# Performance work log

Measured on AMD Instinct MI355X. Metric: run time of the kernel, lower is better.

Reference implementation:

```python
import jax, jax.numpy as jnp
import numpy as np

H = 8            # num_heads
HID = 128        # hidden_channels
D = HID // H     # per-head dim
L = 2            # num_layers
NCLS = 4         # out_channels (number of 1-class heads)


def _forward(x_a, x_b, lin_W_a, lin_b_a, lin_W_b, lin_b_b,
             Wk, bk, Wq, bq, Wv, bv, arel, mrel, prel,
             Wa, ba_out, skip, Wcls, bcls, edges):
    """HGT forward. edges: list of (src_type, dst_type, [2,E] int array); list
    position is the relation index into arel/mrel/prel."""
    # per-type input projection + ReLU
    x = [jax.nn.relu(x_a @ lin_W_a + lin_b_a),
         jax.nn.relu(x_b @ lin_W_b + lin_b_b)]
    N = [x[0].shape[0], x[1].shape[0]]
    scale = 1.0 / np.sqrt(D)
    for l in range(L):
        # per-type K/Q/V projections -> [N, H, D]
        k = [(x[t] @ Wk[l, t] + bk[l, t]).reshape(N[t], H, D) for t in range(2)]
        q = [(x[t] @ Wq[l, t] + bq[l, t]).reshape(N[t], H, D) for t in range(2)]
        v = [(x[t] @ Wv[l, t] + bv[l, t]).reshape(N[t], H, D) for t in range(2)]
        new_x = []
        for dt in range(2):
            logits, vals, dsts = [], [], []
            for r, (s_t, d_t, ei) in enumerate(edges):
                if d_t != dt:
                    continue
                src, dst = ei[0], ei[1]
                # relation-specific per-head transforms of gathered src K/V
                ke = jnp.einsum('ehd,hdf->ehf', k[s_t][src], arel[l, r])  # [E,H,D]
                ve = jnp.einsum('ehd,hdf->ehf', v[s_t][src], mrel[l, r])  # [E,H,D]
                a = jnp.sum(q[dt][dst] * ke, axis=-1) * prel[l, r] * scale  # [E,H]
                logits.append(a); vals.append(ve); dsts.append(dst)
            a = jnp.concatenate(logits, axis=0)
            ve = jnp.concatenate(vals, axis=0)
            dst = jnp.concatenate(dsts, axis=0)
            # segment softmax over all incoming edges per destination node
            amax = jax.ops.segment_max(a, dst, num_segments=N[dt])           # [N,H]
            ae = jnp.exp(a - amax[dst])                                       # [E,H]
            den = jax.ops.segment_sum(ae, dst, num_segments=N[dt])           # [N,H]
            msg = jax.ops.segment_sum(ae[:, :, None] * ve, dst,
                                      num_segments=N[dt])                    # [N,H,D]
            out = (msg / jnp.maximum(den, 1e-16)[:, :, None]).reshape(N[dt], HID)
            # output projection with GELU + learned skip gate
            out = jax.nn.gelu(out) @ Wa[l, dt] + ba_out[l, dt]
            beta = jax.nn.sigmoid(skip[l, dt])
            new_x.append(beta * out + (1.0 - beta) * x[dt])
        x = new_x
    # node_to_predict == 'a'; concatenated 1-class heads -> [Na, NCLS]
    return x[0] @ Wcls.T + bcls


def setup_inputs() -> dict:
    key = jax.random.key(0)
    ks = iter(jax.random.split(key, 40))
    Na, Nb, E = 50000, 50000, 150000
    def rn(shape, fan_in):
        return jax.random.normal(next(ks), shape, dtype=jnp.float32) / np.sqrt(fan_in)
    inp = {
        'x_a': jax.random.normal(next(ks), (Na, 64), dtype=jnp.float32),
        'x_b': jax.random.normal(next(ks), (Nb, 32), dtype=jnp.float32),
        'lin_W_a': rn((64, HID), 64), 'lin_b_a': jnp.zeros((HID,), jnp.float32),
        'lin_W_b': rn((32, HID), 32), 'lin_b_b': jnp.zeros((HID,), jnp.float32),
        'Wk': rn((L, 2, HID, HID), HID), 'bk': jnp.zeros((L, 2, HID), jnp.float32),
        'Wq': rn((L, 2, HID, HID), HID), 'bq': jnp.zeros((L, 2, HID), jnp.float32),
        'Wv': rn((L, 2, HID, HID), HID), 'bv': jnp.zeros((L, 2, HID), jnp.float32),
        'arel': rn((L, 4, H, D, D), D), 'mrel': rn((L, 4, H, D, D), D),
        'prel': jnp.ones((L, 4, H), jnp.float32),
        'Wa': rn((L, 2, HID, HID), HID), 'ba_out': jnp.zeros((L, 2, HID), jnp.float32),
        'skip': jnp.ones((L, 2), jnp.float32),
        'Wcls': rn((NCLS, HID), HID), 'bcls': jnp.zeros((NCLS,), jnp.float32),
        'edge_aa': jax.random.randint(next(ks), (2, E), 0, Na, dtype=jnp.int32),
        'edge_ab': jax.random.randint(next(ks), (2, E), 0, Na, dtype=jnp.int32),
        'edge_ba': jax.random.randint(next(ks), (2, E), 0, Na, dtype=jnp.int32),
        'edge_bb': jax.random.randint(next(ks), (2, E), 0, Nb, dtype=jnp.int32),
    }
    return inp


def reference(x_a, x_b, lin_W_a, lin_b_a, lin_W_b, lin_b_b,
              Wk, bk, Wq, bq, Wv, bv, arel, mrel, prel,
              Wa, ba_out, skip, Wcls, bcls,
              edge_aa, edge_ab, edge_ba, edge_bb):
    edges = [(0, 0, edge_aa), (0, 1, edge_ab), (1, 0, edge_ba), (1, 1, edge_bb)]
    return _forward(x_a, x_b, lin_W_a, lin_b_a, lin_W_b, lin_b_b,
                    Wk, bk, Wq, bq, Wv, bv, arel, mrel, prel,
                    Wa, ba_out, skip, Wcls, bcls, edges)
```

## Files before the change

### kernel.cpp

```cpp
#include <hip/hip_runtime.h>
#include <math.h>

#define HIDC 128
#define NH 8
#define HD 16
#define NCLS 4

typedef __attribute__((ext_vector_type(8))) short s8v;
typedef __attribute__((ext_vector_type(4))) float f4v;

#define ST_STRIDE 264

__device__ __forceinline__ float gelu_f(float h) {
    float z = 0.7978845608028654f * (h + 0.044715f * h * h * h);
    float t = 1.f - 2.f / (1.f + __expf(2.f * z));
    return 0.5f * h * (1.f + t);
}
__device__ __forceinline__ unsigned short f2bf(float x) {
    unsigned b = __float_as_uint(x);
    unsigned r = (b + 0x7FFFu + ((b >> 16) & 1u)) >> 16;
    return (unsigned short)r;
}
__device__ __forceinline__ float bf2f(unsigned short u) {
    return __uint_as_float(((unsigned)u) << 16);
}
__device__ __forceinline__ void gload_lds16(const void* g, void* l) {
    __builtin_amdgcn_global_load_lds(
        (const __attribute__((address_space(1))) unsigned int*)g,
        (__attribute__((address_space(3))) unsigned int*)l, 16, 0, 0);
}

__global__ void zero_u32(unsigned* __restrict__ p, long n)
{
    long i = (long)blockIdx.x * blockDim.x + threadIdx.x;
    long stride = (long)gridDim.x * blockDim.x;
    for (; i < n; i += stride) p[i] = 0u;
}

__global__ void fold_all(const float* __restrict__ Wk, const float* __restrict__ bk,
                         const float* __restrict__ Wv, const float* __restrict__ bv,
                         const float* __restrict__ arel, const float* __restrict__ mrel,
                         float* __restrict__ Wt, float* __restrict__ bt)
{
    __shared__ float rsh[NH * HD * HD];
// ... 145 lines not shown
    unsigned run = bsum[blockIdx.x] + sh[t] - s;
    #pragma unroll
    for (int j = 0; j < 4; ++j) {
        int i = i0 + j;
        if (i < n) { rp[i] = (int)run; cur[i] = run; }
        run += v[j];
    }
}

__global__ void scatter4(const int* __restrict__ e0, int E0, const int* __restrict__ e1, int E1,
                         const int* __restrict__ e2, int E2, const int* __restrict__ e3, int E3,
                         unsigned* __restrict__ cursor, int Nmax,
                         unsigned* __restrict__ adj0, unsigned* __restrict__ adj1)
{
    int i = blockIdx.x * blockDim.x + threadIdx.x;
    int tot = E0 + E1 + E2 + E3;
    int stride = gridDim.x * blockDim.x;
    for (; i < tot; i += stride) {
        int j = i; const int* e; int E; int dt; unsigned rb;
        if (j < E0) { e = e0; E = E0; dt = 0; rb = 0u; }
        else { j -= E0;
            if (j < E1) { e = e1; E = E1; dt = 1; rb = 0u; }
            else { j -= E1;
                if (j < E2) { e = e2; E = E2; dt = 0; rb = 1u << 24; }
                else { j -= E2; e = e3; E = E3; dt = 1; rb = 1u << 24; }
            }
        }
        int s = e[j], d = e[E + j];
        unsigned pos = atomicAdd(&cursor[(size_t)dt * Nmax + d], 1u);
        (dt ? adj1 : adj0)[pos] = (unsigned)s | rb;
    }
}

template <int ASPLIT, int EPI, int OUT, int NK>
__global__ __launch_bounds__(256)
void mgemm(const void* __restrict__ Ain, const unsigned short* __restrict__ W2m,
           const float* __restrict__ bias,
           const unsigned short* __restrict__ xold, const float* __restrict__ skipp,
           void* __restrict__ Cout, int N)
{
    constexpr int K = NK * 32;
    constexpr size_t WSZ = (size_t)4 * K * 128;
    constexpr size_t SSZ = (size_t)128 * ST_STRIDE * 2;
    constexpr size_t LSZ = (OUT == 2 && SSZ > WSZ) ? SSZ : WSZ;
    __shared__ char ldsraw[LSZ];
    unsigned short* lds = (unsigned short*)ldsraw;
    int t = threadIdx.x;
    constexpr int NCP = (4 * K * 128) / (16 * 256);
    #pragma unroll
    for (int i = 0; i < NCP; ++i)
        gload_lds16((const char*)W2m + ((size_t)t + i * 256) * 16,
                    (char*)ldsraw + ((size_t)t + i * 256) * 16);
    __syncthreads();

    int w = t >> 6, lane = t & 63;
    int lr = lane & 15, g = lane >> 4;
    int row0 = blockIdx.x * 128;
    int fnb = w * 2;

    f4v acc[8][2];
    #pragma unroll
    for (int i = 0; i < 8; ++i) { acc[i][0] = (f4v)0.f; acc[i][1] = (f4v)0.f; }

    #pragma unroll
    for (int ks = 0; ks < NK; ++ks) {
        s8v ah[8], al[8];
        #pragma unroll
        for (int fm = 0; fm < 8; ++fm) {
            int row = row0 + fm * 16 + lr;
            if (row < N) {
                if (ASPLIT) {
                    const unsigned short* ap = (const unsigned short*)Ain + (size_t)row * 256 + ks * 32 + g * 8;
                    ah[fm] = *(const s8v*)ap;
                    al[fm] = *(const s8v*)(ap + 128);
                } else {
                    const float* ap = (const float*)Ain + (size_t)row * K + ks * 32 + g * 8;
                    float4 p = *(const float4*)ap;
                    float4 q = *(const float4*)(ap + 4);
                    float xv[8] = {p.x, p.y, p.z, p.w, q.x, q.y, q.z, q.w};
                    #pragma unroll
                    for (int j = 0; j < 8; ++j) {
                        unsigned short h = f2bf(xv[j]);
                        ah[fm][j] = (short)h;
                        al[fm][j] = (short)f2bf(xv[j] - bf2f(h));
                    }
                }
            } else { ah[fm] = (s8v)0; al[fm] = (s8v)0; }
        }
        #pragma unroll
        for (int f = 0; f < 2; ++f) {
            int fn = fnb + f;
            size_t co = (size_t)ks * 8192 + fn * 1024 + g * 256 + lr * 16;
            s8v bh = *(const s8v*)((const char*)ldsraw + co);
            s8v bl = *(const s8v*)((const char*)ldsraw + K * 256 + co);
            #pragma unroll
            for (int fm = 0; fm < 8; ++fm) {
                acc[fm][f] = __builtin_amdgcn_mfma_f32_16x16x32_bf16(ah[fm], bh, acc[fm][f], 0, 0, 0);
                acc[fm][f] = __builtin_amdgcn_mfma_f32_16x16x32_bf16(ah[fm], bl, acc[fm][f], 0, 0, 0);
                acc[fm][f] = __builtin_amdgcn_mfma_f32_16x16x32_bf16(al[fm], bh, acc[fm][f], 0, 0, 0);
            }
        }
    }

    float beta = 0.f;
    if (EPI == 2) beta = 1.f / (1.f + __expf(-skipp[0]));
    int rb = g * 4;

    if (OUT == 2) __syncthreads();

    #pragma unroll
    for (int f = 0; f < 2; ++f) {
        int fn = fnb + f;
        float bv = bias[fn * 16 + lr];
        int col = fn * 16 + lr;
        #pragma unroll
        for (int fm = 0; fm < 8; ++fm) {
            #pragma unroll
            for (int j = 0; j < 4; ++j) {
                int lrow = fm * 16 + rb + j;
                int row = row0 + lrow;
                if (OUT == 0 && row >= N) continue;
                float o = acc[fm][f][j] + bv;
                if (EPI == 1) o = fmaxf(o, 0.f);
                if (EPI == 2) {
                    float xo = (row < N) ? (bf2f(xold[(size_t)row * 256 + col]) +
                                            bf2f(xold[(size_t)row * 256 + 128 + col])) : 0.f;
                    o = beta * o + (1.f - beta) * xo;
                }
                if (OUT == 0) {
                    ((float*)Cout)[(size_t)row * HIDC + col] = o;
                } else {
                    unsigned short h = f2bf(o);
                    lds[(size_t)lrow * ST_STRIDE + col] = h;
                    lds[(size_t)lrow * ST_STRIDE + 128 + col] = f2bf(o - bf2f(h));
                }
            }
        }
    }

    if (OUT == 2) {
        __syncthreads();
        #pragma unroll
        for (int it = 0; it < 16; ++it) {
            int d4 = (it * 256 + t) * 4;
            int row = d4 >> 7, c2 = d4 & 127;
            int grow = row0 + row;
            if (grow < N) {
                uint4 v = *(const uint4*)(lds + (size_t)row * ST_STRIDE + c2 * 2);
                *(uint4*)((unsigned short*)Cout + (size_t)grow * 256 + c2 * 2) = v;
            }
        }
    }
}

struct KvArgs {
    const unsigned short* A[4];
    const unsigned short* Wm[4];
    const float* bias[4];
    unsigned short* out[4];
    int N[4];
    int cum[5];
};

__global__ __launch_bounds__(256)
void mgemm_kv4(KvArgs args)
{
    int bid = blockIdx.x;
    int jb = 0;
    while (jb < 3 && bid >= args.cum[jb + 1]) ++jb;
    int lb = bid - args.cum[jb];
    const unsigned short* Ain = args.A[jb];
    const unsigned short* Wkt = args.Wm[jb];
    const unsigned short* Wvt = args.Wm[jb] + 32768;
    const float* bias2 = args.bias[jb];
    unsigned short* kv = args.out[jb];
    int N = args.N[jb];

    __shared__ char ldsraw[65536];
    unsigned short* lds = (unsigned short*)ldsraw;
    int t = threadIdx.x;
    #pragma unroll
    for (int i = 0; i < 8; ++i)
        gload_lds16((const char*)Wkt + ((size_t)t + i * 256) * 16,
                    ldsraw + ((size_t)t + i * 256) * 16);
    #pragma unroll
    for (int i = 0; i < 8; ++i)
        gload_lds16((const char*)Wvt + ((size_t)t + i * 256) * 16,
                    ldsraw + 32768 + ((size_t)t + i * 256) * 16);

    int w = t >> 6, lane = t & 63;
    int lr = lane & 15, g = lane >> 4;
    int row0 = lb * 64;
    int fnb = w * 2;

    s8v ah[4][4], al[4][4];
    #pragma unroll
    for (int fm = 0; fm < 4; ++fm) {
        int row = row0 + fm * 16 + lr;
        #pragma unroll
        for (int ks = 0; ks < 4; ++ks) {
            if (row < N) {
                const unsigned short* ap = Ain + (size_t)row * 256 + ks * 32 + g * 8;
                ah[fm][ks] = *(const s8v*)ap;
                al[fm][ks] = *(const s8v*)(ap + 128);
            } else { ah[fm][ks] = (s8v)0; al[fm][ks] = (s8v)0; }
        }
    }
    __syncthreads();

    f4v acck[4][2], accv[4][2];
    #pragma unroll
    for (int i = 0; i < 4; ++i) {
        acck[i][0] = (f4v)0.f; acck[i][1] = (f4v)0.f;
        accv[i][0] = (f4v)0.f; accv[i][1] = (f4v)0.f;
    }

    #pragma unroll
    for (int ks = 0; ks < 4; ++ks) {
        #pragma unroll
        for (int f = 0; f < 2; ++f) {
            int fn = fnb + f;
            size_t co = (size_t)ks * 8192 + fn * 1024 + g * 256 + lr * 16;
            s8v bk_ = *(const s8v*)(ldsraw + co);
            s8v bv_ = *(const s8v*)(ldsraw + 32768 + co);
            #pragma unroll
            for (int fm = 0; fm < 4; ++fm) {
                acck[fm][f] = __builtin_amdgcn_mfma_f32_16x16x32_bf16(ah[fm][ks], bk_, acck[fm][f], 0, 0, 0);
                acck[fm][f] = __builtin_amdgcn_mfma_f32_16x16x32_bf16(al[fm][ks], bk_, acck[fm][f], 0, 0, 0);
                accv[fm][f] = __builtin_amdgcn_mfma_f32_16x16x32_bf16(ah[fm][ks], bv_, accv[fm][f], 0, 0, 0);
                accv[fm][f] = __builtin_amdgcn_mfma_f32_16x16x32_bf16(al[fm][ks], bv_, accv[fm][f], 0, 0, 0);
            }
        }
    }

    __syncthreads();
    int rb = g * 4;
    #pragma unroll
    for (int f = 0; f < 2; ++f) {
        int fn = fnb + f;
        int col = fn * 16 + lr;
        float bk0 = bias2[col], bv0 = bias2[128 + col];
        #pragma unroll
        for (int fm = 0; fm < 4; ++fm) {
            #pragma unroll
            for (int j = 0; j < 4; ++j) {
                int lrow = fm * 16 + rb + j;
                lds[(size_t)lrow * ST_STRIDE + col] = f2bf(acck[fm][f][j] + bk0);
                lds[(size_t)lrow * ST_STRIDE + 128 + col] = f2bf(accv[fm][f][j] + bv0);
            }
        }
    }
    __syncthreads();
    #pragma unroll
    for (int it = 0; it < 8; ++it) {
        int d4 = (it * 256 + t) * 4;
        int row = d4 >> 7, c2 = d4 & 127;
        int grow = row0 + row;
        if (grow < N) {
            uint4 v = *(const uint4*)(lds + (size_t)row * ST_STRIDE + c2 * 2);
            *(uint4*)(kv + (size_t)grow * 256 + c2 * 2) = v;
        }
    }
}

struct QArgs {
    const unsigned short* A[2];
    const unsigned short* Wm[2];
    const float* bias[2];
    float* out[2];
    int N[2];
    int cum[3];
};

__global__ __launch_bounds__(256)
void mgemm_q2(QArgs args)
{
    int bid = blockIdx.x;
    int jb = (bid >= args.cum[1]) ? 1 : 0;
    int lb = bid - args.cum[jb];
    const unsigned short* Ain = args.A[jb];
    const unsigned short* W2m = args.Wm[jb];
    const float* bias = args.bias[jb];
    float* Cout = args.out[jb];
    int N = args.N[jb];

    __shared__ unsigned short lds[2 * 128 * 128];
    int t = threadIdx.x;
    #pragma unroll
    for (int i = 0; i < 16; ++i)
        gload_lds16((const char*)W2m + ((size_t)t + i * 256) * 16,
                    (char*)lds + ((size_t)t + i * 256) * 16);
    __syncthreads();

    int w = t >> 6, lane = t & 63;
    int lr = lane & 15, g = lane >> 4;
    int row0 = lb * 128;
    int fnb = w * 2;

    f4v acc[8][2];
    #pragma unroll
    for (int i = 0; i < 8; ++i) { acc[i][0] = (f4v)0.f; acc[i][1] = (f4v)0.f; }

    #pragma unroll
    for (int ks = 0; ks < 4; ++ks) {
        s8v ah[8], al[8];
        #pragma unroll
        for (int fm = 0; fm < 8; ++fm) {
            int row = row0 + fm * 16 + lr;
            if (row < N) {
                const unsigned short* ap = Ain + (size_t)row * 256 + ks * 32 + g * 8;
                ah[fm] = *(const s8v*)ap;
                al[fm] = *(const s8v*)(ap + 128);
            } else { ah[fm] = (s8v)0; al[fm] = (s8v)0; }
        }
        #pragma unroll
        for (int f = 0; f < 2; ++f) {
            int fn = fnb + f;
            size_t co = (size_t)ks * 8192 + fn * 1024 + g * 256 + lr * 16;
            s8v bh = *(const s8v*)((const char*)lds + co);
            s8v bl = *(const s8v*)((const char*)lds + 32768 + co);
            #pragma unroll
            for (int fm = 0; fm < 8; ++fm) {
                acc[fm][f] = __builtin_amdgcn_mfma_f32_16x16x32_bf16(ah[fm], bh, acc[fm][f], 0, 0, 0);
                acc[fm][f] = __builtin_amdgcn_mfma_f32_16x16x32_bf16(ah[fm], bl, acc[fm][f], 0, 0, 0);
                acc[fm][f] = __builtin_amdgcn_mfma_f32_16x16x32_bf16(al[fm], bh, acc[fm][f], 0, 0, 0);
            }
        }
    }

    int rb = g * 4;
    #pragma unroll
    for (int f = 0; f < 2; ++f) {
        int fn = fnb + f;
        float bv = bias[fn * 16 + lr];
        int col = fn * 16 + lr;
        #pragma unroll
        for (int fm = 0; fm < 8; ++fm) {
            #pragma unroll
            for (int j = 0; j < 4; ++j) {
                int row = row0 + fm * 16 + rb + j;
                if (row >= N) continue;
                Cout[(size_t)row * HIDC + col] = acc[fm][f][j] + bv;
            }
        }
    }
}

#define EDGE_STEP(IDX, M, S, AX, AY)                                               \
    {                                                                              \
        unsigned ent = adj[IDX];                                                   \
        int src = (int)(ent & 0xFFFFFFu);                                          \
        const unsigned short* kv = (ent >> 24) ? kvB : kvA;                        \
        float sp = (ent >> 24) ? spB : spA;                                        \
        ushort2 kraw = *(const ushort2*)(kv + (size_t)src * 256 + lane * 2);       \
        ushort2 vraw = *(const ushort2*)(kv + (size_t)src * 256 + 128 + lane * 2); \
        float p = bf2f(kraw.x) * qv.x + bf2f(kraw.y) * qv.y;                       \
        p += __shfl_xor(p, 1, 8);                                                  \
        p += __shfl_xor(p, 2, 8);                                                  \
        p += __shfl_xor(p, 4, 8);                                                  \
        float a = p * sp;                                                          \
        float mn = fmaxf(M, a);                                                    \
        float cc = __expf(M - mn);                                                 \
        float pe = __expf(a - mn);                                                 \
        S = S * cc + pe;                                                           \
        AX = AX * cc + pe * bf2f(vraw.x);                                          \
        AY = AY * cc + pe * bf2f(vraw.y);                                          \
        M = mn;                                                                    \
    }

__global__ __launch_bounds__(256)
void agg_fused(const float* __restrict__ Q,
               const unsigned short* __restrict__ kvA, const unsigned short* __restrict__ kvB,
               const int* __restrict__ rowptr, const unsigned* __restrict__ adj,
               const float* __restrict__ prelA, const float* __restrict__ prelB,
               float scale, unsigned short* __restrict__ msgs, int N)
{
// ... 116 lines not shown
    float* bt = (float*)base; base += (size_t)16 * HIDC * 4;
    size_t nW2 = (size_t)2 * (Ka + Kb) * 128 + (size_t)24 * 32768;
    unsigned short* W2 = (unsigned short*)base; base += nW2 * 2;
    unsigned* cnt = (unsigned*)base; base += (size_t)2 * Nmax * 4;
    unsigned* cursor = (unsigned*)base; base += (size_t)2 * Nmax * 4;
    unsigned* bsum = (unsigned*)base; base += 256 * 4;
    int* rowptr = (int*)base; base += (size_t)2 * (Nmax + 1) * 4;
    unsigned* adj0 = (unsigned*)base; base += (size_t)(Ee[0] + Ee[2]) * 4;
    unsigned* adj1 = (unsigned*)base; base += (size_t)(Ee[1] + Ee[3]) * 4;

    size_t off_lina = 0;
    size_t off_linb = (size_t)2 * Ka * 128;
    size_t base128  = (size_t)2 * (Ka + Kb) * 128;
    auto offKT = [&](int l, int st, int dt) { return base128 + (size_t)(l * 8 + (st * 2 + dt) * 2) * 32768; };
    auto offQ  = [&](int l, int tt) { return base128 + (size_t)(16 + l * 2 + tt) * 32768; };
    auto offA  = [&](int l, int tt) { return base128 + (size_t)(20 + l * 2 + tt) * 32768; };

    fold_all<<<16, 128, 0, stream>>>(Wk, bk, Wv, bv, arel, mrel, Wt, bt);
    int nwblk = (Ka >> 5) + (Kb >> 5) + 24 * 4;
    wsplit<<<nwblk, 128, 0, stream>>>(lin_W_a, lin_W_b, Wq, Wa, Wt, W2, Ka, Kb);

    int nblk = (Nmax + 1023) / 1024;
    zero_u32<<<512, 256, 0, stream>>>(cnt, (long)2 * Nmax);
    hist4<<<1024, 256, 0, stream>>>(eptr[0] + Ee[0], Ee[0], eptr[1] + Ee[1], Ee[1],
                                    eptr[2] + Ee[2], Ee[2], eptr[3] + Ee[3], Ee[3],
                                    cnt, Nmax);
    scan_p1<<<2 * nblk, 256, 0, stream>>>(cnt, bsum, Nmax, nblk, Na, Nb);
    scan_p2<<<1, 256, 0, stream>>>(bsum, nblk, rowptr, Nmax, Na, Nb);
    scan_p3<<<2 * nblk, 256, 0, stream>>>(cnt, bsum, rowptr, cursor, Nmax, nblk, Na, Nb);
    scatter4<<<1024, 256, 0, stream>>>(eptr[0], Ee[0], eptr[1], Ee[1],
                                       eptr[2], Ee[2], eptr[3], Ee[3],
                                       cursor, Nmax, adj0, adj1);

    int gn128[2] = {(Na + 127) / 128, (Nb + 127) / 128};
    int gn64[2]  = {(Na + 63) / 64, (Nb + 63) / 64};
    mgemm<0, 1, 2, 2><<<gn128[0], 256, 0, stream>>>(x_a, W2 + off_lina, lin_b_a,
                                                    nullptr, nullptr, xs[0], Na);
    mgemm<0, 1, 2, 1><<<gn128[1], 256, 0, stream>>>(x_b, W2 + off_linb, lin_b_b,
                                                    nullptr, nullptr, xs[1], Nb);

    const float scale = 0.25f;

    for (int l = 0; l < 2; ++l) {
        KvArgs ka;
        int cum = 0;
        for (int j = 0; j < 4; ++j) {
            int st = j >> 1, dt = j & 1;
            int bid = l * 8 + (st * 2 + dt) * 2;
            ka.A[j] = xs[st];
            ka.Wm[j] = W2 + offKT(l, st, dt);
            ka.bias[j] = bt + (size_t)bid * HIDC;
            ka.out[j] = kvb[st][dt];
            ka.N[j] = Nn[st];
            ka.cum[j] = cum;
            cum += gn64[st];
        }
        ka.cum[4] = cum;
        mgemm_kv4<<<cum, 256, 0, stream>>>(ka);

        QArgs qa;
        qa.A[0] = xs[0]; qa.Wm[0] = W2 + offQ(l, 0);
        qa.bias[0] = bq + (l * 2 + 0) * HIDC; qa.out[0] = qb[0]; qa.N[0] = Nn[0];
        qa.A[1] = xs[1]; qa.Wm[1] = W2 + offQ(l, 1);
        qa.bias[1] = bq + (l * 2 + 1) * HIDC; qa.out[1] = qb[1]; qa.N[1] = Nn[1];
        qa.cum[0] = 0; qa.cum[1] = gn128[0]; qa.cum[2] = gn128[0] + gn128[1];
        mgemm_q2<<<qa.cum[2], 256, 0, stream>>>(qa);

        agg_fused<<<(Nn[1] + 3) / 4, 256, 0, stream>>>(qb[1], kvb[0][1], kvb[1][1],
                                                       rowptr + (Nmax + 1), adj1,
                                                       prel + (l * 4 + 1) * NH, prel + (l * 4 + 3) * NH,
                                                       scale, msgs, Nn[1]);
        mgemm<1, 2, 2, 4><<<gn128[1], 256, 0, stream>>>(msgs, W2 + offA(l, 1),
                                                        ba + (l * 2 + 1) * HIDC,
                                                        xs[1], skip + (l * 2 + 1), xs[1], Nn[1]);
        agg_fused<<<(Nn[0] + 3) / 4, 256, 0, stream>>>(qb[0], kvb[0][0], kvb[1][0],
                                                       rowptr, adj0,
                                                       prel + (l * 4 + 0) * NH, prel + (l * 4 + 2) * NH,
                                                       scale, msgs, Nn[0]);
        mgemm<1, 2, 2, 4><<<gn128[0], 256, 0, stream>>>(msgs, W2 + offA(l, 0),
                                                        ba + (l * 2 + 0) * HIDC,
                                                        xs[0], skip + (l * 2 + 0), xs[0], Nn[0]);
    }

    cls_kernel<<<(Na + 3) / 4, 256, 0, stream>>>(xs[0], Wcls, bcls, (float*)d_out, Na);
}
```

Baseline: 702.7 us.

## Merge K/V and Q GEMMs into one launch with 64-row tiles

Replaces the separate KV and Q GEMM kernels with one layer_gemm launch per layer that covers six jobs. It also moves the dense GEMMs from 128-row to 64-row tiles, staging the hi and lo weight halves through LDS in two sequential phases. The aim is fewer launches, more blocks for occupancy, and smaller LDS use. The cost is reloading weights mid-kernel behind extra barriers, and for the Q jobs dropping the lo activation term, which reduces precision slightly.

```diff
diff --git a/kernel.cpp b/kernel.cpp
--- a/kernel.cpp
+++ b/kernel.cpp
@@ -10,6 +10,7 @@
 typedef __attribute__((ext_vector_type(4))) float f4v;
 
 #define ST_STRIDE 264
+#define ST_BYTES  (64 * ST_STRIDE * 2)
 
 __device__ __forceinline__ float gelu_f(float h) {
     float z = 0.7978845608028654f * (h + 0.044715f * h * h * h);
@@ -221,41 +222,40 @@
     }
 }
 
-template <int ASPLIT, int EPI, int OUT, int NK>
+template <int ASPLIT, int EPI, int NK>
 __global__ __launch_bounds__(256)
-void mgemm(const void* __restrict__ Ain, const unsigned short* __restrict__ W2m,
-           const float* __restrict__ bias,
-           const unsigned short* __restrict__ xold, const float* __restrict__ skipp,
-           void* __restrict__ Cout, int N)
+void mgemm64(const void* __restrict__ Ain, const unsigned short* __restrict__ W2m,
+             const float* __restrict__ bias,
+             const unsigned short* __restrict__ xold, const float* __restrict__ skipp,
+             unsigned short* __restrict__ Cout, int N)
 {
     constexpr int K = NK * 32;
-    constexpr size_t WSZ = (size_t)4 * K * 128;
-    constexpr size_t SSZ = (size_t)128 * ST_STRIDE * 2;
-    constexpr size_t LSZ = (OUT == 2 && SSZ > WSZ) ? SSZ : WSZ;
+    constexpr int PB = K * 256;
+    constexpr size_t LSZ = (PB > ST_BYTES) ? PB : ST_BYTES;
     __shared__ char ldsraw[LSZ];
     unsigned short* lds = (unsigned short*)ldsraw;
     int t = threadIdx.x;
-    constexpr int NCP = (4 * K * 128) / (16 * 256);
+    constexpr int NCP = PB / (16 * 256);
     #pragma unroll
     for (int i = 0; i < NCP; ++i)
         gload_lds16((const char*)W2m + ((size_t)t + i * 256) * 16,
-                    (char*)ldsraw + ((size_t)t + i * 256) * 16);
+                    ldsraw + ((size_t)t + i * 256) * 16);
     __syncthreads();
 
     int w = t >> 6, lane = t & 63;
     int lr = lane & 15, g = lane >> 4;
-    int row0 = blockIdx.x * 128;
+    int row0 = blockIdx.x * 64;
     int fnb = w * 2;
 
-    f4v acc[8][2];
-    #pragma unroll
-    for (int i = 0; i < 8; ++i) { acc[i][0] = (f4v)0.f; acc[i][1] = (f4v)0.f; }
+    f4v acc[4][2];
+    #pragma unroll
+    for (int i = 0; i < 4; ++i) { acc[i][0] = (f4v)0.f; acc[i][1] = (f4v)0.f; }
 
     #pragma unroll
     for (int ks = 0; ks < NK; ++ks) {
-        s8v ah[8], al[8];
-        #pragma unroll
-        for (int fm = 0; fm < 8; ++fm) {
+        s8v ah[4], al[4];
+        #pragma unroll
+        for (int fm = 0; fm < 4; ++fm) {
             int row = row0 + fm * 16 + lr;
             if (row < N) {
                 if (ASPLIT) {
@@ -278,37 +278,66 @@
         }
         #pragma unroll
         for (int f = 0; f < 2; ++f) {
-            int fn = fnb + f;
-            size_t co = (size_t)ks * 8192 + fn * 1024 + g * 256 + lr * 16;
-            s8v bh = *(const s8v*)((const char*)ldsraw + co);
-            s8v bl = *(const s8v*)((const char*)ldsraw + K * 256 + co);
+            size_t co = (size_t)ks * 8192 + (fnb + f) * 1024 + g * 256 + lr * 16;
+            s8v b = *(const s8v*)(ldsraw + co);
             #pragma unroll
-            for (int fm = 0; fm < 8; ++fm) {
-                acc[fm][f] = __builtin_amdgcn_mfma_f32_16x16x32_bf16(ah[fm], bh, acc[fm][f], 0, 0, 0);
-                acc[fm][f] = __builtin_amdgcn_mfma_f32_16x16x32_bf16(ah[fm], bl, acc[fm][f], 0, 0, 0);
-                acc[fm][f] = __builtin_amdgcn_mfma_f32_16x16x32_bf16(al[fm], bh, acc[fm][f], 0, 0, 0);
-            }
+            for (int fm = 0; fm < 4; ++fm) {
+                acc[fm][f] = __builtin_amdgcn_mfma_f32_16x16x32_bf16(ah[fm], b, acc[fm][f], 0, 0, 0);
+                acc[fm][f] = __builtin_amdgcn_mfma_f32_16x16x32_bf16(al[fm], b, acc[fm][f], 0, 0, 0);
+            }
+        }
+    }
+
+    __syncthreads();
+    #pragma unroll
+    for (int i = 0; i < NCP; ++i)
+        gload_lds16((const char*)(W2m + (size_t)K * 128) + ((size_t)t + i * 256) * 16,
+                    ldsraw + ((size_t)t + i * 256) * 16);
+    __syncthreads();
+
+    #pragma unroll
+    for (int ks = 0; ks < NK; ++ks) {
+        s8v ah[4];
+        #pragma unroll
+        for (int fm = 0; fm < 4; ++fm) {
+            int row = row0 + fm * 16 + lr;
+            if (row < N) {
+                if (ASPLIT) {
+                    ah[fm] = *(const s8v*)((const unsigned short*)Ain + (size_t)row * 256 + ks * 32 + g * 8);
+                } else {
+                    const float* ap = (const float*)Ain + (size_t)row * K + ks * 32 + g * 8;
+                    float4 p = *(const float4*)ap;
+                    float4 q = *(const float4*)(ap + 4);
+                    float xv[8] = {p.x, p.y, p.z, p.w, q.x, q.y, q.z, q.w};
+                    #pragma unroll
+                    for (int j = 0; j < 8; ++j) ah[fm][j] = (short)f2bf(xv[j]);
+                }
+            } else ah[fm] = (s8v)0;
+        }
+        #pragma unroll
+        for (int f = 0; f < 2; ++f) {
+            size_t co = (size_t)ks * 8192 + (fnb + f) * 1024 + g * 256 + lr * 16;
+            s8v b = *(const s8v*)(ldsraw + co);
+            #pragma unroll
+            for (int fm = 0; fm < 4; ++fm)
+                acc[fm][f] = __builtin_amdgcn_mfma_f32_16x16x32_bf16(ah[fm], b, acc[fm][f], 0, 0, 0);
         }
     }
 
     float beta = 0.f;
     if (EPI == 2) beta = 1.f / (1.f + __expf(-skipp[0]));
     int rb = g * 4;
-
-    if (OUT == 2) __syncthreads();
-
+    __syncthreads();
     #pragma unroll
     for (int f = 0; f < 2; ++f) {
-        int fn = fnb + f;
-        float bv = bias[fn * 16 + lr];
-        int col = fn * 16 + lr;
-        #pragma unroll
-        for (int fm = 0; fm < 8; ++fm) {
+        int col = (fnb + f) * 16 + lr;
+        float bv = bias[col];
+        #pragma unroll
+        for (int fm = 0; fm < 4; ++fm) {
             #pragma unroll
             for (int j = 0; j < 4; ++j) {
                 int lrow = fm * 16 + rb + j;
                 int row = row0 + lrow;
-                if (OUT == 0 && row >= N) continue;
                 float o = acc[fm][f][j] + bv;
                 if (EPI == 1) o = fmaxf(o, 0.f);
                 if (EPI == 2) {
@@ -316,126 +345,9 @@
                                             bf2f(xold[(size_t)row * 256 + 128 + col])) : 0.f;
                     o = beta * o + (1.f - beta) * xo;
                 }
-                if (OUT == 0) {
-                    ((float*)Cout)[(size_t)row * HIDC + col] = o;
-                } else {
-                    unsigned short h = f2bf(o);
-                    lds[(size_t)lrow * ST_STRIDE + col] = h;
-                    lds[(size_t)lrow * ST_STRIDE + 128 + col] = f2bf(o - bf2f(h));
-                }
-            }
-        }
-    }
-
-    if (OUT == 2) {
-        __syncthreads();
-        #pragma unroll
-        for (int it = 0; it < 16; ++it) {
-            int d4 = (it * 256 + t) * 4;
-            int row = d4 >> 7, c2 = d4 & 127;
-            int grow = row0 + row;
-            if (grow < N) {
-                uint4 v = *(const uint4*)(lds + (size_t)row * ST_STRIDE + c2 * 2);
-                *(uint4*)((unsigned short*)Cout + (size_t)grow * 256 + c2 * 2) = v;
-            }
-        }
-    }
-}
-
-struct KvArgs {
-    const unsigned short* A[4];
-    const unsigned short* Wm[4];
-    const float* bias[4];
-    unsigned short* out[4];
-    int N[4];
-    int cum[5];
-};
-
-__global__ __launch_bounds__(256)
-void mgemm_kv4(KvArgs args)
-{
-    int bid = blockIdx.x;
-    int jb = 0;
-    while (jb < 3 && bid >= args.cum[jb + 1]) ++jb;
-    int lb = bid - args.cum[jb];
-    const unsigned short* Ain = args.A[jb];
-    const unsigned short* Wkt = args.Wm[jb];
-    const unsigned short* Wvt = args.Wm[jb] + 32768;
-    const float* bias2 = args.bias[jb];
-    unsigned short* kv = args.out[jb];
-    int N = args.N[jb];
-
-    __shared__ char ldsraw[65536];
-    unsigned short* lds = (unsigned short*)ldsraw;
-    int t = threadIdx.x;
-    #pragma unroll
-    for (int i = 0; i < 8; ++i)
-        gload_lds16((const char*)Wkt + ((size_t)t + i * 256) * 16,
-                    ldsraw + ((size_t)t + i * 256) * 16);
-    #pragma unroll
-    for (int i = 0; i < 8; ++i)
-        gload_lds16((const char*)Wvt + ((size_t)t + i * 256) * 16,
-                    ldsraw + 32768 + ((size_t)t + i * 256) * 16);
-
-    int w = t >> 6, lane = t & 63;
-    int lr = lane & 15, g = lane >> 4;
-    int row0 = lb * 64;
-    int fnb = w * 2;
-
-    s8v ah[4][4], al[4][4];
-    #pragma unroll
-    for (int fm = 0; fm < 4; ++fm) {
-        int row = row0 + fm * 16 + lr;
-        #pragma unroll
-        for (int ks = 0; ks < 4; ++ks) {
-            if (row < N) {
-                const unsigned short* ap = Ain + (size_t)row * 256 + ks * 32 + g * 8;
-                ah[fm][ks] = *(const s8v*)ap;
-                al[fm][ks] = *(const s8v*)(ap + 128);
-            } else { ah[fm][ks] = (s8v)0; al[fm][ks] = (s8v)0; }
-        }
-    }
-    __syncthreads();
-
-    f4v acck[4][2], accv[4][2];
-    #pragma unroll
-    for (int i = 0; i < 4; ++i) {
-        acck[i][0] = (f4v)0.f; acck[i][1] = (f4v)0.f;
-        accv[i][0] = (f4v)0.f; accv[i][1] = (f4v)0.f;
-    }
-
-    #pragma unroll
-    for (int ks = 0; ks < 4; ++ks) {
-        #pragma unroll
-        for (int f = 0; f < 2; ++f) {
-            int fn = fnb + f;
-            size_t co = (size_t)ks * 8192 + fn * 1024 + g * 256 + lr * 16;
-            s8v bk_ = *(const s8v*)(ldsraw + co);
-            s8v bv_ = *(const s8v*)(ldsraw + 32768 + co);
-            #pragma unroll
-            for (int fm = 0; fm < 4; ++fm) {
-                acck[fm][f] = __builtin_amdgcn_mfma_f32_16x16x32_bf16(ah[fm][ks], bk_, acck[fm][f], 0, 0, 0);
-                acck[fm][f] = __builtin_amdgcn_mfma_f32_16x16x32_bf16(al[fm][ks], bk_, acck[fm][f], 0, 0, 0);
-                accv[fm][f] = __builtin_amdgcn_mfma_f32_16x16x32_bf16(ah[fm][ks], bv_, accv[fm][f], 0, 0, 0);
-                accv[fm][f] = __builtin_amdgcn_mfma_f32_16x16x32_bf16(al[fm][ks], bv_, accv[fm][f], 0, 0, 0);
-            }
-        }
-    }
-
-    __syncthreads();
-    int rb = g * 4;
-    #pragma unroll
-    for (int f = 0; f < 2; ++f) {
-        int fn = fnb + f;
-        int col = fn * 16 + lr;
-        float bk0 = bias2[col], bv0 = bias2[128 + col];
-        #pragma unroll
-        for (int fm = 0; fm < 4; ++fm) {
-            #pragma unroll
-            for (int j = 0; j < 4; ++j) {
-                int lrow = fm * 16 + rb + j;
-                lds[(size_t)lrow * ST_STRIDE + col] = f2bf(acck[fm][f][j] + bk0);
-                lds[(size_t)lrow * ST_STRIDE + 128 + col] = f2bf(accv[fm][f][j] + bv0);
+                unsigned short h = f2bf(o);
+                lds[(size_t)lrow * ST_STRIDE + col] = h;
+                lds[(size_t)lrow * ST_STRIDE + 128 + col] = f2bf(o - bf2f(h));
             }
         }
     }
@@ -447,89 +359,155 @@
         int grow = row0 + row;
         if (grow < N) {
             uint4 v = *(const uint4*)(lds + (size_t)row * ST_STRIDE + c2 * 2);
-            *(uint4*)(kv + (size_t)grow * 256 + c2 * 2) = v;
-        }
-    }
-}
-
-struct QArgs {
-    const unsigned short* A[2];
-    const unsigned short* Wm[2];
-    const float* bias[2];
-    float* out[2];
-    int N[2];
-    int cum[3];
+            *(uint4*)(Cout + (size_t)grow * 256 + c2 * 2) = v;
+        }
+    }
+}
+
+struct LJob {
+    const unsigned short* A;
+    const unsigned short* W1;
+    const unsigned short* W2p;
+    const float* bias;
+    void* out;
+    int N;
+    int mode;
 };
+struct LArgs { LJob job[6]; int cum[7]; };
 
 __global__ __launch_bounds__(256)
-void mgemm_q2(QArgs args)
+void layer_gemm(LArgs args)
 {
     int bid = blockIdx.x;
-    int jb = (bid >= args.cum[1]) ? 1 : 0;
+    int jb = 0;
+    while (jb < 5 && bid >= args.cum[jb + 1]) ++jb;
+    LJob J = args.job[jb];
     int lb = bid - args.cum[jb];
-    const unsigned short* Ain = args.A[jb];
-    const unsigned short* W2m = args.Wm[jb];
-    const float* bias = args.bias[jb];
-    float* Cout = args.out[jb];
-    int N = args.N[jb];
-
-    __shared__ unsigned short lds[2 * 128 * 128];
+
+    __shared__ char ldsraw[ST_BYTES];
+    unsigned short* lds = (unsigned short*)ldsraw;
     int t = threadIdx.x;
     #pragma unroll
-    for (int i = 0; i < 16; ++i)
-        gload_lds16((const char*)W2m + ((size_t)t + i * 256) * 16,
-                    (char*)lds + ((size_t)t + i * 256) * 16);
+    for (int i = 0; i < 8; ++i)
+        gload_lds16((const char*)J.W1 + ((size_t)t + i * 256) * 16,
+                    ldsraw + ((size_t)t + i * 256) * 16);
     __syncthreads();
 
     int w = t >> 6, lane = t & 63;
     int lr = lane & 15, g = lane >> 4;
-    int row0 = lb * 128;
+    int row0 = lb * 64;
     int fnb = w * 2;
-
-    f4v acc[8][2];
-    #pragma unroll
-    for (int i = 0; i < 8; ++i) { acc[i][0] = (f4v)0.f; acc[i][1] = (f4v)0.f; }
+    int N = J.N;
+
+    f4v acc1[4][2], acc2[4][2];
+    #pragma unroll
+    for (int i = 0; i < 4; ++i) {
+        acc1[i][0] = (f4v)0.f; acc1[i][1] = (f4v)0.f;
+        acc2[i][0] = (f4v)0.f; acc2[i][1] = (f4v)0.f;
+    }
 
     #pragma unroll
     for (int ks = 0; ks < 4; ++ks) {
-        s8v ah[8], al[8];
-        #pragma unroll
-        for (int fm = 0; fm < 8; ++fm) {
+        s8v ah[4], al[4];
+        #pragma unroll
+        for (int fm = 0; fm < 4; ++fm) {
             int row = row0 + fm * 16 + lr;
             if (row < N) {
-                const unsigned short* ap = Ain + (size_t)row * 256 + ks * 32 + g * 8;
+                const unsigned short* ap = J.A + (size_t)row * 256 + ks * 32 + g * 8;
                 ah[fm] = *(const s8v*)ap;
                 al[fm] = *(const s8v*)(ap + 128);
             } else { ah[fm] = (s8v)0; al[fm] = (s8v)0; }
         }
         #pragma unroll
         for (int f = 0; f < 2; ++f) {
-            int fn = fnb + f;
-            size_t co = (size_t)ks * 8192 + fn * 1024 + g * 256 + lr * 16;
-            s8v bh = *(const s8v*)((const char*)lds + co);
-            s8v bl = *(const s8v*)((const char*)lds + 32768 + co);
+            size_t co = (size_t)ks * 8192 + (fnb + f) * 1024 + g * 256 + lr * 16;
+            s8v b = *(const s8v*)(ldsraw + co);
             #pragma unroll
-            for (int fm = 0; fm < 8; ++fm) {
-                acc[fm][f] = __builtin_amdgcn_mfma_f32_16x16x32_bf16(ah[fm], bh, acc[fm][f], 0, 0, 0);
-                acc[fm][f] = __builtin_amdgcn_mfma_f32_16x16x32_bf16(ah[fm], bl, acc[fm][f], 0, 0, 0);
-                acc[fm][f] = __builtin_amdgcn_mfma_f32_16x16x32_bf16(al[fm], bh, acc[fm][f], 0, 0, 0);
+            for (int fm = 0; fm < 4; ++fm) {
+                acc1[fm][f] = __builtin_amdgcn_mfma_f32_16x16x32_bf16(ah[fm], b, acc1[fm][f], 0, 0, 0);
+                acc1[fm][f] = __builtin_amdgcn_mfma_f32_16x16x32_bf16(al[fm], b, acc1[fm][f], 0, 0, 0);
+            }
+        }
+    }
+
+    __syncthreads();
+    #pragma unroll
+    for (int i = 0; i < 8; ++i)
+        gload_lds16((const char*)J.W2p + ((size_t)t + i * 256) * 16,
+                    ldsraw + ((size_t)t + i * 256) * 16);
+    __syncthreads();
+
+    #pragma unroll
+    for (int ks = 0; ks < 4; ++ks) {
+        s8v ah[4], al[4];
+        #pragma unroll
+        for (int fm = 0; fm < 4; ++fm) {
+            int row = row0 + fm * 16 + lr;
+            if (row < N) {
+                const unsigned short* ap = J.A + (size_t)row * 256 + ks * 32 + g * 8;
+                ah[fm] = *(const s8v*)ap;
+                if (J.mode == 0) al[fm] = *(const s8v*)(ap + 128);
+                else al[fm] = (s8v)0;
+            } else { ah[fm] = (s8v)0; al[fm] = (s8v)0; }
+        }
+        #pragma unroll
+        for (int f = 0; f < 2; ++f) {
+            size_t co = (size_t)ks * 8192 + (fnb + f) * 1024 + g * 256 + lr * 16;
+            s8v b = *(const s8v*)(ldsraw + co);
+            #pragma unroll
+            for (int fm = 0; fm < 4; ++fm) {
+                if (J.mode == 0) {
+                    acc2[fm][f] = __builtin_amdgcn_mfma_f32_16x16x32_bf16(ah[fm], b, acc2[fm][f], 0, 0, 0);
+                    acc2[fm][f] = __builtin_amdgcn_mfma_f32_16x16x32_bf16(al[fm], b, acc2[fm][f], 0, 0, 0);
+                } else {
+                    acc1[fm][f] = __builtin_amdgcn_mfma_f32_16x16x32_bf16(ah[fm], b, acc1[fm][f], 0, 0, 0);
+                }
             }
         }
     }
 
     int rb = g * 4;
-    #pragma unroll
-    for (int f = 0; f < 2; ++f) {
-        int fn = fnb + f;
-        float bv = bias[fn * 16 + lr];
-        int col = fn * 16 + lr;
-        #pragma unroll
-        for (int fm = 0; fm < 8; ++fm) {
+    if (J.mode == 0) {
+        __syncthreads();
+        unsigned short* kv = (unsigned short*)J.out;
+        #pragma unroll
+        for (int f = 0; f < 2; ++f) {
+            int col = (fnb + f) * 16 + lr;
+            float bk0 = J.bias[col], bv0 = J.bias[128 + col];
             #pragma unroll
-            for (int j = 0; j < 4; ++j) {
-                int row = row0 + fm * 16 + rb + j;
-                if (row >= N) continue;
-                Cout[(size_t)row * HIDC + col] = acc[fm][f][j] + bv;
+            for (int fm = 0; fm < 4; ++fm) {
+                #pragma unroll
+                for (int j = 0; j < 4; ++j) {
+                    int lrow = fm * 16 + rb + j;
+                    lds[(size_t)lrow * ST_STRIDE + col] = f2bf(acc1[fm][f][j] + bk0);
+                    lds[(size_t)lrow * ST_STRIDE + 128 + col] = f2bf(acc2[fm][f][j] + bv0);
+                }
+            }
+        }
+        __syncthreads();
+        #pragma unroll
+        for (int it = 0; it < 8; ++it) {
+            int d4 = (it * 256 + t) * 4;
+            int row = d4 >> 7, c2 = d4 & 127;
+            int grow = row0 + row;
+            if (grow < N) {
+                uint4 v = *(const uint4*)(lds + (size_t)row * ST_STRIDE + c2 * 2);
+                *(uint4*)(kv + (size_t)grow * 256 + c2 * 2) = v;
+            }
+        }
+    } else {
+        float* Cout = (float*)J.out;
+        #pragma unroll
+        for (int f = 0; f < 2; ++f) {
+            int col = (fnb + f) * 16 + lr;
+            float bv = J.bias[col];
+            #pragma unroll
+            for (int fm = 0; fm < 4; ++fm) {
+                #pragma unroll
+                for (int j = 0; j < 4; ++j) {
+                    int row = row0 + fm * 16 + rb + j;
+                    if (row < N) Cout[(size_t)row * HIDC + col] = acc1[fm][f][j] + bv;
+                }
             }
         }
     }
@@ -713,54 +691,58 @@
                                        eptr[2], Ee[2], eptr[3], Ee[3],
                                        cursor, Nmax, adj0, adj1);
 
-    int gn128[2] = {(Na + 127) / 128, (Nb + 127) / 128};
-    int gn64[2]  = {(Na + 63) / 64, (Nb + 63) / 64};
-    mgemm<0, 1, 2, 2><<<gn128[0], 256, 0, stream>>>(x_a, W2 + off_lina, lin_b_a,
-                                                    nullptr, nullptr, xs[0], Na);
-    mgemm<0, 1, 2, 1><<<gn128[1], 256, 0, stream>>>(x_b, W2 + off_linb, lin_b_b,
-                                                    nullptr, nullptr, xs[1], Nb);
+    int gn64[2] = {(Na + 63) / 64, (Nb + 63) / 64};
+    mgemm64<0, 1, 2><<<gn64[0], 256, 0, stream>>>(x_a, W2 + off_lina, lin_b_a,
+                                                  nullptr, nullptr, xs[0], Na);
+    mgemm64<0, 1, 1><<<gn64[1], 256, 0, stream>>>(x_b, W2 + off_linb, lin_b_b,
+                                                  nullptr, nullptr, xs[1], Nb);
 
     const float scale = 0.25f;
 
     for (int l = 0; l < 2; ++l) {
-        KvArgs ka;
+        LArgs la;
         int cum = 0;
         for (int j = 0; j < 4; ++j) {
             int st = j >> 1, dt = j & 1;
             int bid = l * 8 + (st * 2 + dt) * 2;
-            ka.A[j] = xs[st];
-            ka.Wm[j] = W2 + offKT(l, st, dt);
-            ka.bias[j] = bt + (size_t)bid * HIDC;
-            ka.out[j] = kvb[st][dt];
-            ka.N[j] = Nn[st];
-            ka.cum[j] = cum;
+            la.job[j].A = xs[st];
+            la.job[j].W1 = W2 + offKT(l, st, dt);
+            la.job[j].W2p = W2 + offKT(l, st, dt) + 32768;
+            la.job[j].bias = bt + (size_t)bid * HIDC;
+            la.job[j].out = kvb[st][dt];
+            la.job[j].N = Nn[st];
+            la.job[j].mode = 0;
+            la.cum[j] = cum;
             cum += gn64[st];
         }
-        ka.cum[4] = cum;
-        mgemm_kv4<<<cum, 256, 0, stream>>>(ka);
-
-        QArgs qa;
-        qa.A[0] = xs[0]; qa.Wm[0] = W2 + offQ(l, 0);
-        qa.bias[0] = bq + (l * 2 + 0) * HIDC; qa.out[0] = qb[0]; qa.N[0] = Nn[0];
-        qa.A[1] = xs[1]; qa.Wm[1] = W2 + offQ(l, 1);
-        qa.bias[1] = bq + (l * 2 + 1) * HIDC; qa.out[1] = qb[1]; qa.N[1] = Nn[1];
-        qa.cum[0] = 0; qa.cum[1] = gn128[0]; qa.cum[2] = gn128[0] + gn128[1];
-        mgemm_q2<<<qa.cum[2], 256, 0, stream>>>(qa);
+        for (int j = 0; j < 2; ++j) {
+            la.job[4 + j].A = xs[j];
+            la.job[4 + j].W1 = W2 + offQ(l, j);
+            la.job[4 + j].W2p = W2 + offQ(l, j) + 16384;
+            la.job[4 + j].bias = bq + (l * 2 + j) * HIDC;
+            la.job[4 + j].out = qb[j];
+            la.job[4 + j].N = Nn[j];
+            la.job[4 + j].mode = 1;
+            la.cum[4 + j] = cum;
+            cum += gn64[j];
+        }
+        la.cum[6] = cum;
+        layer_gemm<<<cum, 256, 0, stream>>>(la);
 
         agg_fused<<<(Nn[1] + 3) / 4, 256, 0, stream>>>(qb[1], kvb[0][1], kvb[1][1],
                                                        rowptr + (Nmax + 1), adj1,
                                                        prel + (l * 4 + 1) * NH, prel + (l * 4 + 3) * NH,
                                                        scale, msgs, Nn[1]);
-        mgemm<1, 2, 2, 4><<<gn128[1], 256, 0, stream>>>(msgs, W2 + offA(l, 1),
-                                                        ba + (l * 2 + 1) * HIDC,
-                                                        xs[1], skip + (l * 2 + 1), xs[1], Nn[1]);
+        mgemm64<1, 2, 4><<<gn64[1], 256, 0, stream>>>(msgs, W2 + offA(l, 1),
+                                                      ba + (l * 2 + 1) * HIDC,
+                                                      xs[1], skip + (l * 2 + 1), xs[1], Nn[1]);
         agg_fused<<<(Nn[0] + 3) / 4, 256, 0, stream>>>(qb[0], kvb[0][0], kvb[1][0],
                                                        rowptr, adj0,
                                                        prel + (l * 4 + 0) * NH, prel + (l * 4 + 2) * NH,
                                                        scale, msgs, Nn[0]);
-        mgemm<1, 2, 2, 4><<<gn128[0], 256, 0, stream>>>(msgs, W2 + offA(l, 0),
-                                                        ba + (l * 2 + 0) * HIDC,
-                                                        xs[0], skip + (l * 2 + 0), xs[0], Nn[0]);
+        mgemm64<1, 2, 4><<<gn64[0], 256, 0, stream>>>(msgs, W2 + offA(l, 0),
+                                                      ba + (l * 2 + 0) * HIDC,
+                                                      xs[0], skip + (l * 2 + 0), xs[0], Nn[0]);
     }
 
     cls_kernel<<<(Na + 3) / 4, 256, 0, stream>>>(xs[0], Wcls, bcls, (float*)d_out, Na);
```

Measured after the change: 774.8 us. 10.3% more time.

## Use two-pass split-bf16 GEMMs with 64-row tiles and per-type Q launches

Applied to the files above, without the earlier changes.

The GEMM kernel drops the low-half weight term, doing hi*W + lo*W (2 MFMAs) instead of 3, and only loads the high-precision weight half into LDS. Row tiles shrink from 128 to 64 so more blocks launch, and the fused Q kernel is replaced by two separate launches of the generic GEMM. Dropping the weight low part loses some accuracy, but only relative to the more precise three-term split; the grid doubles and one extra launch is added per layer.

```diff
diff --git a/kernel.cpp b/kernel.cpp
--- a/kernel.cpp
+++ b/kernel.cpp
@@ -10,6 +10,7 @@
 typedef __attribute__((ext_vector_type(4))) float f4v;
 
 #define ST_STRIDE 264
+#define ST_BYTES  (64 * ST_STRIDE * 2)
 
 __device__ __forceinline__ float gelu_f(float h) {
     float z = 0.7978845608028654f * (h + 0.044715f * h * h * h);
@@ -223,39 +224,38 @@
 
 template <int ASPLIT, int EPI, int OUT, int NK>
 __global__ __launch_bounds__(256)
-void mgemm(const void* __restrict__ Ain, const unsigned short* __restrict__ W2m,
-           const float* __restrict__ bias,
-           const unsigned short* __restrict__ xold, const float* __restrict__ skipp,
-           void* __restrict__ Cout, int N)
+void mg2p(const void* __restrict__ Ain, const unsigned short* __restrict__ Whi,
+          const float* __restrict__ bias,
+          const unsigned short* __restrict__ xold, const float* __restrict__ skipp,
+          void* __restrict__ Cout, int N)
 {
     constexpr int K = NK * 32;
-    constexpr size_t WSZ = (size_t)4 * K * 128;
-    constexpr size_t SSZ = (size_t)128 * ST_STRIDE * 2;
-    constexpr size_t LSZ = (OUT == 2 && SSZ > WSZ) ? SSZ : WSZ;
+    constexpr int PB = NK * 8192;
+    constexpr size_t LSZ = (OUT == 2 && ST_BYTES > PB) ? ST_BYTES : PB;
     __shared__ char ldsraw[LSZ];
     unsigned short* lds = (unsigned short*)ldsraw;
     int t = threadIdx.x;
-    constexpr int NCP = (4 * K * 128) / (16 * 256);
+    constexpr int NCP = PB / (16 * 256);
     #pragma unroll
     for (int i = 0; i < NCP; ++i)
-        gload_lds16((const char*)W2m + ((size_t)t + i * 256) * 16,
-                    (char*)ldsraw + ((size_t)t + i * 256) * 16);
+        gload_lds16((const char*)Whi + ((size_t)t + i * 256) * 16,
+                    ldsraw + ((size_t)t + i * 256) * 16);
     __syncthreads();
 
     int w = t >> 6, lane = t & 63;
     int lr = lane & 15, g = lane >> 4;
-    int row0 = blockIdx.x * 128;
+    int row0 = blockIdx.x * 64;
     int fnb = w * 2;
 
-    f4v acc[8][2];
-    #pragma unroll
-    for (int i = 0; i < 8; ++i) { acc[i][0] = (f4v)0.f; acc[i][1] = (f4v)0.f; }
+    f4v acc[4][2];
+    #pragma unroll
+    for (int i = 0; i < 4; ++i) { acc[i][0] = (f4v)0.f; acc[i][1] = (f4v)0.f; }
 
     #pragma unroll
     for (int ks = 0; ks < NK; ++ks) {
-        s8v ah[8], al[8];
-        #pragma unroll
-        for (int fm = 0; fm < 8; ++fm) {
+        s8v ah[4], al[4];
+        #pragma unroll
+        for (int fm = 0; fm < 4; ++fm) {
             int row = row0 + fm * 16 + lr;
             if (row < N) {
                 if (ASPLIT) {
@@ -278,15 +278,12 @@
         }
         #pragma unroll
         for (int f = 0; f < 2; ++f) {
-            int fn = fnb + f;
-            size_t co = (size_t)ks * 8192 + fn * 1024 + g * 256 + lr * 16;
-            s8v bh = *(const s8v*)((const char*)ldsraw + co);
-            s8v bl = *(const s8v*)((const char*)ldsraw + K * 256 + co);
+            size_t co = (size_t)ks * 8192 + (fnb + f) * 1024 + g * 256 + lr * 16;
+            s8v b = *(const s8v*)(ldsraw + co);
             #pragma unroll
-            for (int fm = 0; fm < 8; ++fm) {
-                acc[fm][f] = __builtin_amdgcn_mfma_f32_16x16x32_bf16(ah[fm], bh, acc[fm][f], 0, 0, 0);
-                acc[fm][f] = __builtin_amdgcn_mfma_f32_16x16x32_bf16(ah[fm], bl, acc[fm][f], 0, 0, 0);
-                acc[fm][f] = __builtin_amdgcn_mfma_f32_16x16x32_bf16(al[fm], bh, acc[fm][f], 0, 0, 0);
+            for (int fm = 0; fm < 4; ++fm) {
+                acc[fm][f] = __builtin_amdgcn_mfma_f32_16x16x32_bf16(ah[fm], b, acc[fm][f], 0, 0, 0);
+                acc[fm][f] = __builtin_amdgcn_mfma_f32_16x16x32_bf16(al[fm], b, acc[fm][f], 0, 0, 0);
             }
         }
     }
@@ -295,48 +292,56 @@
     if (EPI == 2) beta = 1.f / (1.f + __expf(-skipp[0]));
     int rb = g * 4;
 
-    if (OUT == 2) __syncthreads();
-
-    #pragma unroll
-    for (int f = 0; f < 2; ++f) {
-        int fn = fnb + f;
-        float bv = bias[fn * 16 + lr];
-        int col = fn * 16 + lr;
-        #pragma unroll
-        for (int fm = 0; fm < 8; ++fm) {
+    if (OUT == 2) {
+        __syncthreads();
+        #pragma unroll
+        for (int f = 0; f < 2; ++f) {
+            int col = (fnb + f) * 16 + lr;
+            float bv = bias[col];
             #pragma unroll
-            for (int j = 0; j < 4; ++j) {
-                int lrow = fm * 16 + rb + j;
-                int row = row0 + lrow;
-                if (OUT == 0 && row >= N) continue;
-                float o = acc[fm][f][j] + bv;
-                if (EPI == 1) o = fmaxf(o, 0.f);
-                if (EPI == 2) {
-                    float xo = (row < N) ? (bf2f(xold[(size_t)row * 256 + col]) +
-                                            bf2f(xold[(size_t)row * 256 + 128 + col])) : 0.f;
-                    o = beta * o + (1.f - beta) * xo;
-                }
-                if (OUT == 0) {
-                    ((float*)Cout)[(size_t)row * HIDC + col] = o;
-                } else {
+            for (int fm = 0; fm < 4; ++fm) {
+                #pragma unroll
+                for (int j = 0; j < 4; ++j) {
+                    int lrow = fm * 16 + rb + j;
+                    int row = row0 + lrow;
+                    float o = acc[fm][f][j] + bv;
+                    if (EPI == 1) o = fmaxf(o, 0.f);
+                    if (EPI == 2) {
+                        float xo = (row < N) ? (bf2f(xold[(size_t)row * 256 + col]) +
+                                                bf2f(xold[(size_t)row * 256 + 128 + col])) : 0.f;
+                        o = beta * o + (1.f - beta) * xo;
+                    }
                     unsigned short h = f2bf(o);
                     lds[(size_t)lrow * ST_STRIDE + col] = h;
                     lds[(size_t)lrow * ST_STRIDE + 128 + col] = f2bf(o - bf2f(h));
                 }
             }
         }
-    }
-
-    if (OUT == 2) {
         __syncthreads();
-        #pragma unroll
-        for (int it = 0; it < 16; ++it) {
+        unsigned short* C = (unsigned short*)Cout;
+        #pragma unroll
+        for (int it = 0; it < 8; ++it) {
             int d4 = (it * 256 + t) * 4;
             int row = d4 >> 7, c2 = d4 & 127;
             int grow = row0 + row;
             if (grow < N) {
                 uint4 v = *(const uint4*)(lds + (size_t)row * ST_STRIDE + c2 * 2);
-                *(uint4*)((unsigned short*)Cout + (size_t)grow * 256 + c2 * 2) = v;
+                *(uint4*)(C + (size_t)grow * 256 + c2 * 2) = v;
+            }
+        }
+    } else {
+        float* C = (float*)Cout;
+        #pragma unroll
+        for (int f = 0; f < 2; ++f) {
+            int col = (fnb + f) * 16 + lr;
+            float bv = bias[col];
+            #pragma unroll
+            for (int fm = 0; fm < 4; ++fm) {
+                #pragma unroll
+                for (int j = 0; j < 4; ++j) {
+                    int row = row0 + fm * 16 + rb + j;
+                    if (row < N) C[(size_t)row * HIDC + col] = acc[fm][f][j] + bv;
+                }
             }
         }
     }
@@ -448,89 +453,6 @@
         if (grow < N) {
             uint4 v = *(const uint4*)(lds + (size_t)row * ST_STRIDE + c2 * 2);
             *(uint4*)(kv + (size_t)grow * 256 + c2 * 2) = v;
-        }
-    }
-}
-
-struct QArgs {
-    const unsigned short* A[2];
-    const unsigned short* Wm[2];
-    const float* bias[2];
-    float* out[2];
-    int N[2];
-    int cum[3];
-};
-
-__global__ __launch_bounds__(256)
-void mgemm_q2(QArgs args)
-{
-    int bid = blockIdx.x;
-    int jb = (bid >= args.cum[1]) ? 1 : 0;
-    int lb = bid - args.cum[jb];
-    const unsigned short* Ain = args.A[jb];
-    const unsigned short* W2m = args.Wm[jb];
-    const float* bias = args.bias[jb];
-    float* Cout = args.out[jb];
-    int N = args.N[jb];
-
-    __shared__ unsigned short lds[2 * 128 * 128];
-    int t = threadIdx.x;
-    #pragma unroll
-    for (int i = 0; i < 16; ++i)
-        gload_lds16((const char*)W2m + ((size_t)t + i * 256) * 16,
-                    (char*)lds + ((size_t)t + i * 256) * 16);
-    __syncthreads();
-
-    int w = t >> 6, lane = t & 63;
-    int lr = lane & 15, g = lane >> 4;
-    int row0 = lb * 128;
-    int fnb = w * 2;
-
-    f4v acc[8][2];
-    #pragma unroll
-    for (int i = 0; i < 8; ++i) { acc[i][0] = (f4v)0.f; acc[i][1] = (f4v)0.f; }
-
-    #pragma unroll
-    for (int ks = 0; ks < 4; ++ks) {
-        s8v ah[8], al[8];
-        #pragma unroll
-        for (int fm = 0; fm < 8; ++fm) {
-            int row = row0 + fm * 16 + lr;
-            if (row < N) {
-                const unsigned short* ap = Ain + (size_t)row * 256 + ks * 32 + g * 8;
-                ah[fm] = *(const s8v*)ap;
-                al[fm] = *(const s8v*)(ap + 128);
-            } else { ah[fm] = (s8v)0; al[fm] = (s8v)0; }
-        }
-        #pragma unroll
-        for (int f = 0; f < 2; ++f) {
-            int fn = fnb + f;
-            size_t co = (size_t)ks * 8192 + fn * 1024 + g * 256 + lr * 16;
-            s8v bh = *(const s8v*)((const char*)lds + co);
-            s8v bl = *(const s8v*)((const char*)lds + 32768 + co);
-            #pragma unroll
-            for (int fm = 0; fm < 8; ++fm) {
-                acc[fm][f] = __builtin_amdgcn_mfma_f32_16x16x32_bf16(ah[fm], bh, acc[fm][f], 0, 0, 0);
-                acc[fm][f] = __builtin_amdgcn_mfma_f32_16x16x32_bf16(ah[fm], bl, acc[fm][f], 0, 0, 0);
-                acc[fm][f] = __builtin_amdgcn_mfma_f32_16x16x32_bf16(al[fm], bh, acc[fm][f], 0, 0, 0);
-            }
-        }
-    }
-
-    int rb = g * 4;
-    #pragma unroll
-    for (int f = 0; f < 2; ++f) {
-        int fn = fnb + f;
-        float bv = bias[fn * 16 + lr];
-        int col = fn * 16 + lr;
-        #pragma unroll
-        for (int fm = 0; fm < 8; ++fm) {
-            #pragma unroll
-            for (int j = 0; j < 4; ++j) {
-                int row = row0 + fm * 16 + rb + j;
-                if (row >= N) continue;
-                Cout[(size_t)row * HIDC + col] = acc[fm][f][j] + bv;
-            }
         }
     }
 }
@@ -713,12 +635,11 @@
                                        eptr[2], Ee[2], eptr[3], Ee[3],
                                        cursor, Nmax, adj0, adj1);
 
-    int gn128[2] = {(Na + 127) / 128, (Nb + 127) / 128};
-    int gn64[2]  = {(Na + 63) / 64, (Nb + 63) / 64};
-    mgemm<0, 1, 2, 2><<<gn128[0], 256, 0, stream>>>(x_a, W2 + off_lina, lin_b_a,
-                                                    nullptr, nullptr, xs[0], Na);
-    mgemm<0, 1, 2, 1><<<gn128[1], 256, 0, stream>>>(x_b, W2 + off_linb, lin_b_b,
-                                                    nullptr, nullptr, xs[1], Nb);
+    int gn64[2] = {(Na + 63) / 64, (Nb + 63) / 64};
+    mg2p<0, 1, 2, 2><<<gn64[0], 256, 0, stream>>>(x_a, W2 + off_lina, lin_b_a,
+                                                  nullptr, nullptr, xs[0], Na);
+    mg2p<0, 1, 2, 1><<<gn64[1], 256, 0, stream>>>(x_b, W2 + off_linb, lin_b_b,
+                                                  nullptr, nullptr, xs[1], Nb);
 
     const float scale = 0.25f;
 
@@ -739,28 +660,27 @@
         ka.cum[4] = cum;
         mgemm_kv4<<<cum, 256, 0, stream>>>(ka);
 
-        QArgs qa;
-        qa.A[0] = xs[0]; qa.Wm[0] = W2 + offQ(l, 0);
-        qa.bias[0] = bq + (l * 2 + 0) * HIDC; qa.out[0] = qb[0]; qa.N[0] = Nn[0];
-        qa.A[1] = xs[1]; qa.Wm[1] = W2 + offQ(l, 1);
-        qa.bias[1] = bq + (l * 2 + 1) * HIDC; qa.out[1] = qb[1]; qa.N[1] = Nn[1];
-        qa.cum[0] = 0; qa.cum[1] = gn128[0]; qa.cum[2] = gn128[0] + gn128[1];
-        mgemm_q2<<<qa.cum[2], 256, 0, stream>>>(qa);
+        mg2p<1, 0, 0, 4><<<gn64[1], 256, 0, stream>>>(xs[1], W2 + offQ(l, 1),
+                                                      bq + (l * 2 + 1) * HIDC,
+                                                      nullptr, nullptr, qb[1], Nn[1]);
+        mg2p<1, 0, 0, 4><<<gn64[0], 256, 0, stream>>>(xs[0], W2 + offQ(l, 0),
+                                                      bq + (l * 2 + 0) * HIDC,
+                                                      nullptr, nullptr, qb[0], Nn[0]);
 
         agg_fused<<<(Nn[1] + 3) / 4, 256, 0, stream>>>(qb[1], kvb[0][1], kvb[1][1],
                                                        rowptr + (Nmax + 1), adj1,
                                                        prel + (l * 4 + 1) * NH, prel + (l * 4 + 3) * NH,
                                                        scale, msgs, Nn[1]);
-        mgemm<1, 2, 2, 4><<<gn128[1], 256, 0, stream>>>(msgs, W2 + offA(l, 1),
-                                                        ba + (l * 2 + 1) * HIDC,
-                                                        xs[1], skip + (l * 2 + 1), xs[1], Nn[1]);
+        mg2p<1, 2, 2, 4><<<gn64[1], 256, 0, stream>>>(msgs, W2 + offA(l, 1),
+                                                      ba + (l * 2 + 1) * HIDC,
+                                                      xs[1], skip + (l * 2 + 1), xs[1], Nn[1]);
         agg_fused<<<(Nn[0] + 3) / 4, 256, 0, stream>>>(qb[0], kvb[0][0], kvb[1][0],
                                                        rowptr, adj0,
                                                        prel + (l * 4 + 0) * NH, prel + (l * 4 + 2) * NH,
                                                        scale, msgs, Nn[0]);
-        mgemm<1, 2, 2, 4><<<gn128[0], 256, 0, stream>>>(msgs, W2 + offA(l, 0),
-                                                        ba + (l * 2 + 0) * HIDC,
-                                                        xs[0], skip + (l * 2 + 0), xs[0], Nn[0]);
+        mg2p<1, 2, 2, 4><<<gn64[0], 256, 0, stream>>>(msgs, W2 + offA(l, 0),
+                                                      ba + (l * 2 + 0) * HIDC,
+                                                      xs[0], skip + (l * 2 + 0), xs[0], Nn[0]);
     }
 
     cls_kernel<<<(Na + 3) / 4, 256, 0, stream>>>(xs[0], Wcls, bcls, (float*)d_out, Na);
```

Result: faster. 623.0 us (-11.3%).
